# Performance work log

Measured on AMD Instinct MI355X. Metric: run time of the kernel, lower is better.

## Reference

```python
import jax, jax.numpy as jnp
import numpy as np

B, S, D = 4, 2048, 2048
NQ, NKV = 16, 4
HD = D // NQ          # head_size = 128
GROUP = NQ // NKV     # 4


def _rope_table(seq_len, head_size, theta=10000.0):
    # [seq, head_size/2, 2] = (cos, sin), matching torch polar freqs_cis
    inv = 1.0 / (theta ** (np.arange(0, head_size, 2, dtype=np.float32) / head_size))
    ang = np.arange(seq_len, dtype=np.float32)[:, None] * inv[None, :]
    return jnp.asarray(np.stack([np.cos(ang), np.sin(ang)], axis=-1))


def setup_inputs() -> dict:
    key = jax.random.key(0)
    ks = jax.random.split(key, 6)
    sd = 0.02
    return {
        "x": jax.random.normal(ks[0], (B, S, D), jnp.float32),
        "freq_cis": _rope_table(S, HD),
        "Wq": jax.random.normal(ks[1], (D, NQ * HD), jnp.float32) * sd,
        "bq": jnp.zeros((NQ * HD,), jnp.float32),
        "Wk": jax.random.normal(ks[2], (D, NKV * HD), jnp.float32) * sd,
        "bk": jnp.zeros((NKV * HD,), jnp.float32),
        "Wv": jax.random.normal(ks[3], (D, NKV * HD), jnp.float32) * sd,
        "bv": jnp.zeros((NKV * HD,), jnp.float32),
        "Wo": jax.random.normal(ks[4], (NQ * HD, D), jnp.float32) * sd,
        "start_pos": 0,
    }


def _apply_rope(x, fc):
    # x: [b, s, h, d]; fc: [s, d/2, 2] -> complex multiply on (even, odd) pairs
    xr = x.reshape(*x.shape[:-1], -1, 2)
    cos = fc[None, :, None, :, 0]
    sin = fc[None, :, None, :, 1]
    x0, x1 = xr[..., 0], xr[..., 1]
    out = jnp.stack([x0 * cos - x1 * sin, x0 * sin + x1 * cos], axis=-1)
    return out.reshape(x.shape)


def reference(x, freq_cis, Wq, bq, Wk, bk, Wv, bv, Wo, start_pos):
    b, s, _ = x.shape
    q = (x @ Wq + bq).reshape(b, s, NQ, HD)
    k = (x @ Wk + bk).reshape(b, s, NKV, HD)
    v = (x @ Wv + bv).reshape(b, s, NKV, HD)

    fc = freq_cis[start_pos:start_pos + s]
    q = _apply_rope(q, fc)
    k = _apply_rope(k, fc)

    # [b, nkv, group, s, d] query view; k/v stay [b, nkv, s, d] (GQA broadcast)
    q = q.transpose(0, 2, 1, 3).reshape(b, NKV, GROUP, s, HD)
    k = k.transpose(0, 2, 1, 3)
    v = v.transpose(0, 2, 1, 3)

    scale = 1.0 / jnp.sqrt(jnp.asarray(HD, x.dtype))
    scores = jnp.einsum("bhgqd,bhkd->bhgqk", q, k) * scale
    causal = jnp.tril(jnp.ones((s, s), bool))
    scores = jnp.where(causal[None, None, None], scores, jnp.asarray(-jnp.inf, scores.dtype))
    probs = jax.nn.softmax(scores, axis=-1)
    o = jnp.einsum("bhgqk,bhkd->bhgqd", probs, v)

    o = o.reshape(b, NQ, s, HD).transpose(0, 2, 1, 3).reshape(b, s, NQ * HD)
    return o @ Wo
```

## Files before the change

### kernel.cpp

```cpp
#include <hip/hip_runtime.h>
#include <stdint.h>

typedef __attribute__((ext_vector_type(8))) short bf16x8;
typedef __attribute__((ext_vector_type(4))) float f32x4;
typedef __attribute__((ext_vector_type(16))) float f32x16;

#define S_LEN 2048
#define D_MODEL 2048
#define NQH 16
#define NKVH 4
#define HDIM 128
#define BATCH 4

__device__ __forceinline__ float bf2f(unsigned short s) {
  union { unsigned u; float f; } v; v.u = ((unsigned)s) << 16; return v.f;
}
__device__ __forceinline__ unsigned short f2bf(float f) {
  union { float f; unsigned u; } v; v.f = f;
  unsigned r = v.u + 0x7FFFu + ((v.u >> 16) & 1u);
  return (unsigned short)(r >> 16);
}
__device__ __forceinline__ f32x4 fzero() {
  f32x4 v; v[0]=0.f; v[1]=0.f; v[2]=0.f; v[3]=0.f; return v;
}
__device__ __forceinline__ void async16(const void* g, void* l) {
  __builtin_amdgcn_global_load_lds(
      (const __attribute__((address_space(1))) unsigned int*)g,
      (__attribute__((address_space(3))) unsigned int*)l, 16, 0, 0);
}
__device__ __forceinline__ unsigned cvtpk(float lo, float hi) {
  unsigned r;
  asm("v_cvt_pk_bf16_f32 %0, %1, %2" : "=v"(r) : "v"(lo), "v"(hi));
  return r;
}

__global__ void k_convert_x(const float* __restrict__ x, unsigned short* __restrict__ xb, int n4) {
  int stride = gridDim.x * blockDim.x;
  for (int i = blockIdx.x * blockDim.x + threadIdx.x; i < n4; i += stride) {
    float4 v = ((const float4*)x)[i];
    ushort4 o;
    o.x = f2bf(v.x); o.y = f2bf(v.y); o.z = f2bf(v.z); o.w = f2bf(v.w);
    ((ushort4*)xb)[i] = o;
  }
}

__global__ void k_transpose_convert(const float* __restrict__ W, unsigned short* __restrict__ Wt,
                                    int K, int N) {
  __shared__ float tile[32][33];
  int tx = threadIdx.x & 31, ty = threadIdx.x >> 5;
  int n0 = blockIdx.x * 32, k0 = blockIdx.y * 32;
  #pragma unroll
  for (int i = 0; i < 4; ++i)
    tile[ty + i*8][tx] = W[(size_t)(k0 + ty + i*8) * N + n0 + tx];
  __syncthreads();
  #pragma unroll
  for (int i = 0; i < 4; ++i)
    Wt[(size_t)(n0 + ty + i*8) * K + k0 + tx] = f2bf(tile[tx][ty + i*8]);
}

__global__ void k_transpose_bf16(const unsigned short* __restrict__ src,
                                 unsigned short* __restrict__ dst, int R, int C) {
  __shared__ unsigned short tile[32][33];
  int tx = threadIdx.x & 31, ty = threadIdx.x >> 5;
  int c0 = blockIdx.x * 32, r0 = blockIdx.y * 32;
  const unsigned short* s = src + (size_t)blockIdx.z * R * C;
  unsigned short* d = dst + (size_t)blockIdx.z * R * C;
  #pragma unroll
  for (int i = 0; i < 4; ++i)
    tile[ty + i*8][tx] = s[(size_t)(r0 + ty + i*8) * C + c0 + tx];
  __syncthreads();
  #pragma unroll
  for (int i = 0; i < 4; ++i)
    d[(size_t)(c0 + ty + i*8) * R + r0 + tx] = tile[tx][ty + i*8];
}

#define BARRIER() __builtin_amdgcn_s_barrier()
#define LGKM0()  do { asm volatile("s_waitcnt lgkmcnt(0)" ::: "memory"); \
                      __builtin_amdgcn_sched_barrier(0); } while (0)
#define VMCNT6() asm volatile("s_waitcnt vmcnt(6)" ::: "memory")
#define VMCNT4() asm volatile("s_waitcnt vmcnt(4)" ::: "memory")
#define VMCNT0() asm volatile("s_waitcnt vmcnt(0)" ::: "memory")

__device__ __forceinline__ bf16x8 ldsrd(const unsigned short* L, int row, int kk, int g) {
  int Xs = (kk * 64 + g * 16) ^ ((row & 7) << 4);
  return *(const bf16x8*)&L[row * 64 + (Xs >> 1)];
}
__device__ __forceinline__ void stage8(const unsigned short* __restrict__ G, int gbase,
                                       int k0, unsigned short* lds, int rowbase, int lane) {
  int row = rowbase + (lane >> 3);
  int col8 = (lane & 7) ^ ((lane >> 3) & 7);
  async16(G + (size_t)(gbase + row) * 2048 + k0 + col8 * 8, lds + rowbase * 64 + lane * 8);
}

__global__ __launch_bounds__(512, 2) void k_gemm_qkv(
    const unsigned short* __restrict__ A, const unsigned short* __restrict__ Bt,
    const float* __restrict__ bq, const float* __restrict__ bk, const float* __restrict__ bv,
    const float* __restrict__ fc, const int* __restrict__ start_pos,
    unsigned short* __restrict__ Qo, unsigned short* __restrict__ Ko, unsigned short* __restrict__ Vo)
{
  __shared__ __align__(16) unsigned short Ab[3][256 * 64];
  __shared__ __align__(16) unsigned short Bb[3][128 * 64];
  const int NT = 32, NXT = 24;
  const int tid = threadIdx.x, lane = tid & 63, w = tid >> 6;
  const int lr = lane & 15, g = lane >> 4;
  const int wm = w >> 2, wn = w & 3;

  int nwg = NXT * 32;
  int cpx = nwg >> 3;
  int bid = blockIdx.x;
  int swz = (bid & 7) * cpx + (bid >> 3);
  const int by = swz / NXT, bx = swz % NXT;
  const int mbase = by * 256, nbase = bx * 128;

  #define ST_A(tt) { unsigned short* L = Ab[(tt) % 3]; int k0 = (tt) * 64; \
    _Pragma("unroll") for (int it = 0; it < 4; ++it) { int c = tid + it * 512; \
      int row = c >> 3, col8 = (c & 7) ^ (row & 7); \
      async16(A + (size_t)(mbase + row) * 2048 + k0 + col8 * 8, L + c * 8); } }
  #define ST_B(tt) { unsigned short* L = Bb[(tt) % 3]; int k0 = (tt) * 64; \
    _Pragma("unroll") for (int it = 0; it < 2; ++it) { int c = tid + it * 512; \
      int row = c >> 3, col8 = (c & 7) ^ (row & 7); \
      async16(Bt + (size_t)(nbase + row) * 2048 + k0 + col8 * 8, L + c * 8); } }

  f32x4 acc[8][2];
  #pragma unroll
  for (int m = 0; m < 8; ++m)
    #pragma unroll
    for (int n = 0; n < 2; ++n) acc[m][n] = fzero();

  ST_A(0); ST_B(0); ST_A(1); ST_B(1);
  VMCNT6();
  BARRIER();

  for (int t = 0; t < NT; ++t) {
    const unsigned short* Al = Ab[t % 3];
    const unsigned short* Bl = Bb[t % 3];
    bf16x8 a[2][4], b[2][2];

    #pragma unroll
    for (int kk = 0; kk < 2; ++kk) {
      #pragma unroll
      for (int m = 0; m < 4; ++m) a[kk][m] = ldsrd(Al, wm * 128 + m * 16 + lr, kk, g);
      #pragma unroll
      for (int n = 0; n < 2; ++n) b[kk][n] = ldsrd(Bl, wn * 32 + n * 16 + lr, kk, g);
    }
    if (t + 2 < NT) ST_A(t + 2);
    BARRIER(); LGKM0();
    __builtin_amdgcn_s_setprio(1);
    #pragma unroll
    for (int kk = 0; kk < 2; ++kk)
      #pragma unroll
      for (int m = 0; m < 4; ++m)
        #pragma unroll
        for (int n = 0; n < 2; ++n)
          acc[m][n] = __builtin_amdgcn_mfma_f32_16x16x32_bf16(a[kk][m], b[kk][n], acc[m][n], 0, 0, 0);
    __builtin_amdgcn_s_setprio(0);
    BARRIER();

    #pragma unroll
    for (int kk = 0; kk < 2; ++kk)
      #pragma unroll
      for (int m = 0; m < 4; ++m) a[kk][m] = ldsrd(Al, wm * 128 + 64 + m * 16 + lr, kk, g);
    if (t + 2 < NT) { ST_B(t + 2); VMCNT6(); } else { VMCNT0(); }
    BARRIER(); LGKM0();
    __builtin_amdgcn_s_setprio(1);
    #pragma unroll
    for (int kk = 0; kk < 2; ++kk)
      #pragma unroll
      for (int m = 0; m < 4; ++m)
        #pragma unroll
        for (int n = 0; n < 2; ++n)
          acc[4 + m][n] = __builtin_amdgcn_mfma_f32_16x16x32_bf16(a[kk][m], b[kk][n], acc[4 + m][n], 0, 0, 0);
    __builtin_amdgcn_s_setprio(0);
    BARRIER();
  }

  const int sp = start_pos[0];
  #pragma unroll
  for (int n = 0; n < 2; ++n) {
    const int ng = nbase + wn * 32 + n * 16 + lr;
    unsigned short* dst;
    int NH; float bias;
    if (ng < 2048)      { dst = Qo; NH = NQH;  bias = bq[ng]; }
    else if (ng < 2560) { dst = Ko; NH = NKVH; bias = bk[ng - 2048]; }
    else                { dst = Vo; NH = NKVH; bias = bv[ng - 2560]; }
    const int hh = (ng < 2048 ? ng : (ng < 2560 ? ng - 2048 : ng - 2560)) >> 7;
    const int dd = ng & 127;
    const bool dorope = (ng < 2560);
    const size_t hoff = (size_t)hh * S_LEN * HDIM + dd;
    const int d2 = dd >> 1;
    #pragma unroll
    for (int m = 0; m < 8; ++m)
      #pragma unroll
      for (int i = 0; i < 4; ++i) {
        int mg = mbase + wm * 128 + (m >> 2) * 64 + (m & 3) * 16 + g * 4 + i;
        int bb = mg >> 11, s = mg & 2047;
        float val = acc[m][n][i] + bias;
        float other = __shfl_xor(val, 1);
        if (dorope) {
          float2 cs = *(const float2*)&fc[((size_t)(sp + s) * 64 + d2) * 2];
          val = (dd & 1) ? fmaf(other, cs.y, val * cs.x)
                         : (val * cs.x - other * cs.y);
        }
        dst[(size_t)bb * NH * S_LEN * HDIM + hoff + (size_t)s * HDIM] = f2bf(val);
      }
  }
  #undef ST_A
  #undef ST_B
}

__global__ __launch_bounds__(512, 2) void k_gemm_out256(
    const unsigned short* __restrict__ A, const unsigned short* __restrict__ Bt,
    float* __restrict__ Cf)
{
  __shared__ __align__(16) unsigned short Abuf[2][256 * 64];
  __shared__ __align__(16) unsigned short Bbuf[2][256 * 64];
  const int NT = 32, NXT = 8;
  const int tid = threadIdx.x, lane = tid & 63, w = tid >> 6;
  const int lr = lane & 15, g = lane >> 4;
  const int wm = w >> 2, wn = w & 3;

  int nwg = NXT * 32;
  int cpx = nwg >> 3;
  int bid = blockIdx.x;
  int swz = (bid & 7) * cpx + (bid >> 3);
  const int by = swz / NXT, bx = swz % NXT;
  const int mbase = by * 256, nbase = bx * 256;

  #define ST_AQ02(tt) if ((tt) < NT) { unsigned short* L = Abuf[(tt) & 1]; int k0 = (tt) * 64; \
    _Pragma("unroll") for (int it = 0; it < 2; ++it) { int sub = it * 8 + w; \
      stage8(A, mbase, k0, L, (sub >> 3) * 128 + (sub & 7) * 8, lane); } }
  #define ST_AQ13(tt) if ((tt) < NT) { unsigned short* L = Abuf[(tt) & 1]; int k0 = (tt) * 64; \
    _Pragma("unroll") for (int it = 0; it < 2; ++it) { int sub = it * 8 + w; \
      stage8(A, mbase, k0, L, 64 + (sub >> 3) * 128 + (sub & 7) * 8, lane); } }
  #define ST_BS0(tt) if ((tt) < NT) { unsigned short* L = Bbuf[(tt) & 1]; int k0 = (tt) * 64; \
    _Pragma("unroll") for (int it = 0; it < 2; ++it) { int sub = it * 8 + w; \
      stage8(Bt, nbase, k0, L, (sub >> 2) * 64 + (sub & 3) * 8, lane); } }
  #define ST_BS1(tt) if ((tt) < NT) { unsigned short* L = Bbuf[(tt) & 1]; int k0 = (tt) * 64; \
    _Pragma("unroll") for (int it = 0; it < 2; ++it) { int sub = it * 8 + w; \
      stage8(Bt, nbase, k0, L, 32 + (sub >> 2) * 64 + (sub & 3) * 8, lane); } }

  f32x4 acc[8][4];
  #pragma unroll
  for (int m = 0; m < 8; ++m)
    #pragma unroll
    for (int n = 0; n < 4; ++n) acc[m][n] = fzero();

  ST_AQ02(0); ST_AQ13(0); ST_BS0(0); ST_BS1(0);
  ST_AQ02(1); ST_BS1(1);
  VMCNT4();
  BARRIER();

  bf16x8 a[2][4], b[2][2];

  for (int t = 0; t < NT; ++t) {
    const unsigned short* Al = Abuf[t & 1];
    const unsigned short* Bl = Bbuf[t & 1];

    #pragma unroll
    for (int kk = 0; kk < 2; ++kk) {
      #pragma unroll
      for (int m = 0; m < 4; ++m) a[kk][m] = ldsrd(Al, wm * 128 + m * 16 + lr, kk, g);
      #pragma unroll
      for (int n = 0; n < 2; ++n) b[kk][n] = ldsrd(Bl, wn * 64 + n * 16 + lr, kk, g);
    }
    ST_AQ13(t + 1);
    BARRIER(); LGKM0();
    __builtin_amdgcn_s_setprio(1);
    #pragma unroll
    for (int kk = 0; kk < 2; ++kk)
      #pragma unroll
      for (int m = 0; m < 4; ++m)
        #pragma unroll
        for (int n = 0; n < 2; ++n)
          acc[m][n] = __builtin_amdgcn_mfma_f32_16x16x32_bf16(a[kk][m], b[kk][n], acc[m][n], 0, 0, 0);
    __builtin_amdgcn_s_setprio(0);
    BARRIER();

    #pragma unroll
    for (int kk = 0; kk < 2; ++kk)
      #pragma unroll
      for (int n = 0; n < 2; ++n) b[kk][n] = ldsrd(Bl, wn * 64 + (2 + n) * 16 + lr, kk, g);
    ST_BS0(t + 1);
    BARRIER(); LGKM0();
    __builtin_amdgcn_s_setprio(1);
    #pragma unroll
    for (int kk = 0; kk < 2; ++kk)
      #pragma unroll
      for (int m = 0; m < 4; ++m)
        #pragma unroll
        for (int n = 0; n < 2; ++n)
          acc[m][2 + n] = __builtin_amdgcn_mfma_f32_16x16x32_bf16(a[kk][m], b[kk][n], acc[m][2 + n], 0, 0, 0);
    __builtin_amdgcn_s_setprio(0);
    BARRIER();

    #pragma unroll
    for (int kk = 0; kk < 2; ++kk)
      #pragma unroll
      for (int m = 0; m < 4; ++m) a[kk][m] = ldsrd(Al, wm * 128 + 64 + m * 16 + lr, kk, g);
    ST_AQ02(t + 2);
    BARRIER(); LGKM0();
    __builtin_amdgcn_s_setprio(1);
    #pragma unroll
    for (int kk = 0; kk < 2; ++kk)
      #pragma unroll
      for (int m = 0; m < 4; ++m)
        #pragma unroll
        for (int n = 0; n < 2; ++n)
          acc[4 + m][2 + n] = __builtin_amdgcn_mfma_f32_16x16x32_bf16(a[kk][m], b[kk][n], acc[4 + m][2 + n], 0, 0, 0);
    __builtin_amdgcn_s_setprio(0);
    BARRIER();

    #pragma unroll
    for (int kk = 0; kk < 2; ++kk)
      #pragma unroll
      for (int n = 0; n < 2; ++n) b[kk][n] = ldsrd(Bl, wn * 64 + n * 16 + lr, kk, g);
    ST_BS1(t + 2);
    VMCNT4();
    BARRIER(); LGKM0();
    __builtin_amdgcn_s_setprio(1);
    #pragma unroll
    for (int kk = 0; kk < 2; ++kk)
      #pragma unroll
      for (int m = 0; m < 4; ++m)
        #pragma unroll
        for (int n = 0; n < 2; ++n)
          acc[4 + m][n] = __builtin_amdgcn_mfma_f32_16x16x32_bf16(a[kk][m], b[kk][n], acc[4 + m][n], 0, 0, 0);
    __builtin_amdgcn_s_setprio(0);
    BARRIER();
  }

  #pragma unroll
  for (int m = 0; m < 8; ++m)
    #pragma unroll
    for (int n = 0; n < 4; ++n)
      #pragma unroll
      for (int i = 0; i < 4; ++i) {
        int mg = mbase + wm * 128 + m * 16 + g * 4 + i;
        int ng = nbase + wn * 64 + n * 16 + lr;
        Cf[(size_t)mg * 2048 + ng] = acc[m][n][i];
      }
  #undef ST_AQ02
  #undef ST_AQ13
  #undef ST_BS0
  #undef ST_BS1
}

__global__ __launch_bounds__(512, 2) void k_flash2(
    const unsigned short* __restrict__ Q, const unsigned short* __restrict__ K,
    const unsigned short* __restrict__ Vt, unsigned short* __restrict__ O)
{
  __shared__ __align__(16) unsigned short SH[32768];

  const int tid = threadIdx.x;
  const int lane = tid & 63;
  const int w = tid >> 6;
  const int ql = lane & 31;
  const int hi = lane >> 5;

  const int bh = blockIdx.x >> 2;
  const int tp = blockIdx.x & 3;
  const int b = bh >> 4, h = bh & 15;
  const int kh = h >> 2;

  const unsigned short* Qbase = Q + (size_t)(b * NQH + h) * S_LEN * HDIM;
  const unsigned short* Kbase = K + (size_t)(b * NKVH + kh) * S_LEN * HDIM;
  const unsigned short* Vtb   = Vt + (size_t)(b * NKVH + kh) * HDIM * S_LEN;

  const float scale = 0.08838834764831845f;

  #pragma unroll 1
  for (int half = 0; half < 2; ++half) {
    const int t = half ? (7 - tp) : tp;
    const int nkv = 4 * t + 4;
    const int qg = t * 256 + w * 32 + ql;

    __syncthreads();

    bf16x8 qf[8];
    {
      const unsigned short* qp = Qbase + (size_t)qg * HDIM;
      #pragma unroll
      for (int dd = 0; dd < 8; ++dd)
        qf[dd] = *(const bf16x8*)(qp + dd * 16 + hi * 8);
    }

    float m_r = -1e30f, l_r = 0.f;
    f32x16 oA[4];
    #pragma unroll
    for (int db = 0; db < 4; ++db)
      #pragma unroll
      for (int r = 0; r < 16; ++r) oA[db][r] = 0.f;

    {
      unsigned short* Kd = SH;
      unsigned short* Vd = SH + 16384;
      #pragma unroll
      for (int it = 0; it < 2; ++it) {
        int c = tid + it * 512;
        int row = c >> 4, col = c & 15;
        int lcol = (col & 8) | ((col ^ (row & 7)) & 7);
        async16(Kbase + (size_t)row * HDIM + lcol * 8, Kd + c * 8);
      }
      #pragma unroll
      for (int it = 0; it < 2; ++it) {
        int c = tid + it * 512;
        int row = c >> 3, col = c & 7;
        int lcol = col ^ (row & 7);
        async16(Vtb + (size_t)row * S_LEN + lcol * 8, Vd + c * 8);
      }
    }
    __syncthreads();

    for (int j = 0; j < nkv; ++j) {
      const int cur = j & 1;
      const unsigned short* Kl = SH + cur * 8192;
      const unsigned short* Vl = SH + 16384 + cur * 8192;

      if (j + 1 < nkv) {
        unsigned short* Kd = SH + (cur ^ 1) * 8192;
        unsigned short* Vd = SH + 16384 + (cur ^ 1) * 8192;
        #pragma unroll
        for (int it = 0; it < 2; ++it) {
          int c = tid + it * 512;
          int row = c >> 4, col = c & 15;
          int lcol = (col & 8) | ((col ^ (row & 7)) & 7);
          async16(Kbase + (size_t)((j + 1) * 64 + row) * HDIM + lcol * 8, Kd + c * 8);
        }
        #pragma unroll
        for (int it = 0; it < 2; ++it) {
          int c = tid + it * 512;
          int row = c >> 3, col = c & 7;
          int lcol = col ^ (row & 7);
          async16(Vtb + (size_t)row * S_LEN + (j + 1) * 64 + lcol * 8, Vd + c * 8);
        }
      }

      if (j * 64 <= t * 256 + w * 32 + 31) {
        f32x16 p0, p1;
        #pragma unroll
        for (int r = 0; r < 16; ++r) { p0[r] = 0.f; p1[r] = 0.f; }
        #pragma unroll
        for (int dd = 0; dd < 8; ++dd) {
          const int off = (((dd * 32 + hi * 16) ^ ((ql & 7) << 4)) >> 1);
          bf16x8 a0 = *(const bf16x8*)&Kl[ql * 128 + off];
          bf16x8 a1 = *(const bf16x8*)&Kl[(32 + ql) * 128 + off];
          p0 = __builtin_amdgcn_mfma_f32_32x32x16_bf16(a0, qf[dd], p0, 0, 0, 0);
          p1 = __builtin_amdgcn_mfma_f32_32x32x16_bf16(a1, qf[dd], p1, 0, 0, 0);
        }

        #pragma unroll
        for (int r = 0; r < 16; ++r) {
          const int kl = (r & 3) + 8 * (r >> 2);
          int kg = j * 64 + kl + 4 * hi;
          p0[r] = (kg > qg) ? -1e30f : p0[r] * scale;
          p1[r] = (kg + 32 > qg) ? -1e30f : p1[r] * scale;
        }

        float pm = -1e30f;
        #pragma unroll
        for (int r = 0; r < 16; ++r) pm = fmaxf(pm, fmaxf(p0[r], p1[r]));
        pm = fmaxf(pm, __shfl_xor(pm, 32));
        const float mn = fmaxf(m_r, pm);
        const float corr = __expf(m_r - mn);
        m_r = mn;
        float rs = 0.f;
        #pragma unroll
        for (int r = 0; r < 16; ++r) {
          p0[r] = __expf(p0[r] - mn);
          p1[r] = __expf(p1[r] - mn);
          rs += p0[r] + p1[r];
        }
        rs += __shfl_xor(rs, 32);
        l_r = l_r * corr + rs;
        #pragma unroll
        for (int db = 0; db < 4; ++db)
          #pragma unroll
          for (int r = 0; r < 16; ++r) oA[db][r] *= corr;

        bf16x8 pb[4];
        {
          unsigned Wv[8], W2v[8];
          #pragma unroll
          for (int d = 0; d < 4; ++d) {
            Wv[d]      = cvtpk(p0[4*d],     p0[4*d + 1]);
            W2v[d]     = cvtpk(p0[4*d + 2], p0[4*d + 3]);
            Wv[4 + d]  = cvtpk(p1[4*d],     p1[4*d + 1]);
            W2v[4 + d] = cvtpk(p1[4*d + 2], p1[4*d + 3]);
          }
          #pragma unroll
          for (int kt = 0; kt < 2; ++kt) {
            #pragma unroll
            for (int s = 0; s < 2; ++s) {
              unsigned ownW   = hi ? Wv[kt*4 + 2*s + 1]  : Wv[kt*4 + 2*s];
              unsigned sendW  = hi ? Wv[kt*4 + 2*s]      : Wv[kt*4 + 2*s + 1];
              unsigned recvW  = (unsigned)__shfl_xor((int)sendW, 32);
              unsigned ownW2  = hi ? W2v[kt*4 + 2*s + 1] : W2v[kt*4 + 2*s];
              unsigned sendW2 = hi ? W2v[kt*4 + 2*s]     : W2v[kt*4 + 2*s + 1];
              unsigned recvW2 = (unsigned)__shfl_xor((int)sendW2, 32);
              union { unsigned u[4]; bf16x8 v; } pk;
              pk.u[0] = hi ? recvW  : ownW;
              pk.u[1] = hi ? recvW2 : ownW2;
              pk.u[2] = hi ? ownW   : recvW;
              pk.u[3] = hi ? ownW2  : recvW2;
              pb[kt*2 + s] = pk.v;
            }
          }
        }

        #pragma unroll
        for (int ks = 0; ks < 4; ++ks) {
          #pragma unroll
          for (int db = 0; db < 4; ++db) {
            const int off = (((ks * 32 + hi * 16) ^ ((ql & 7) << 4)) >> 1);
            bf16x8 av = *(const bf16x8*)&Vl[(db * 32 + ql) * 64 + off];
            oA[db] = __builtin_amdgcn_mfma_f32_32x32x16_bf16(av, pb[ks], oA[db], 0, 0, 0);
          }
        }
      }
      __syncthreads();
    }

    {
      const float invl = 1.f / l_r;
      const int qloc = w * 32 + ql;
      #pragma unroll
      for (int db = 0; db < 4; ++db)
        #pragma unroll
        for (int g4 = 0; g4 < 4; ++g4) {
          unsigned lo  = cvtpk(oA[db][g4*4 + 0] * invl, oA[db][g4*4 + 1] * invl);
          unsigned hi2 = cvtpk(oA[db][g4*4 + 2] * invl, oA[db][g4*4 + 3] * invl);
          int byteoff = qloc * 256 + ((db * 64 + g4 * 16 + hi * 8) ^ ((qloc & 7) << 4));
          *(uint2*)((char*)SH + byteoff) = make_uint2(lo, hi2);
        }
    }
    __syncthreads();
    {
      const int q2 = tid >> 1, hf = tid & 1;
      unsigned short* orow = O + ((size_t)(b * S_LEN + t * 256 + q2)) * D_MODEL + h * HDIM + hf * 64;
      #pragma unroll
      for (int u = 0; u < 8; ++u) {
        int byteoff = q2 * 256 + ((hf * 128 + u * 16) ^ ((q2 & 7) << 4));
        bf16x8 v = *(const bf16x8*)((const char*)SH + byteoff);
        *(bf16x8*)(orow + u * 8) = v;
      }
    }
  }
}

extern "C" void kernel_launch(void* const* d_in, const int* in_sizes, int n_in,
                              void* d_out, int out_size, void* d_ws, size_t ws_size,
                              hipStream_t stream) {
  (void)in_sizes; (void)n_in; (void)out_size; (void)ws_size;
  const float* x  = (const float*)d_in[0];
  const float* fc = (const float*)d_in[1];
  const float* Wq = (const float*)d_in[2];
  const float* bq = (const float*)d_in[3];
  const float* Wk = (const float*)d_in[4];
  const float* bk = (const float*)d_in[5];
  const float* Wv = (const float*)d_in[6];
  const float* bv = (const float*)d_in[7];
  const float* Wo = (const float*)d_in[8];
  const int* start_pos = (const int*)d_in[9];
  float* out = (float*)d_out;

  unsigned short* ws = (unsigned short*)d_ws;
  size_t off = 0;
  unsigned short* xb  = ws + off; off += (size_t)8192 * 2048;
  unsigned short* Wt  = ws + off; off += (size_t)3072 * 2048;
  unsigned short* Wot = ws + off; off += (size_t)2048 * 2048;
  unsigned short* Qb  = ws + off; off += (size_t)BATCH * NQH  * S_LEN * HDIM;
  unsigned short* Kb  = ws + off; off += (size_t)BATCH * NKVH * S_LEN * HDIM;
  unsigned short* Vb  = ws + off; off += (size_t)BATCH * NKVH * S_LEN * HDIM;
  unsigned short* Vtb = ws + off; off += (size_t)BATCH * NKVH * S_LEN * HDIM;
  unsigned short* Ob  = ws + off; off += (size_t)8192 * 2048;

  k_convert_x<<<2048, 256, 0, stream>>>(x, xb, 8192 * 2048 / 4);
  k_transpose_convert<<<dim3(64, 64), 256, 0, stream>>>(Wq, Wt, 2048, 2048);
  k_transpose_convert<<<dim3(16, 64), 256, 0, stream>>>(Wk, Wt + (size_t)2048 * 2048, 2048, 512);
  k_transpose_convert<<<dim3(16, 64), 256, 0, stream>>>(Wv, Wt + (size_t)2560 * 2048, 2048, 512);
  k_transpose_convert<<<dim3(64, 64), 256, 0, stream>>>(Wo, Wot, 2048, 2048);

  k_gemm_qkv<<<dim3(768), 512, 0, stream>>>(xb, Wt, bq, bk, bv, fc, start_pos, Qb, Kb, Vb);

  k_transpose_bf16<<<dim3(4, 64, 16), 256, 0, stream>>>(Vb, Vtb, S_LEN, HDIM);

  k_flash2<<<dim3(256), 512, 0, stream>>>(Qb, Kb, Vtb, Ob);

  k_gemm_out256<<<dim3(256), 512, 0, stream>>>(Ob, Wot, out);
}
```

Baseline: 389.5 us.

## Write V transposed from QKV GEMM, split RoPE out, lazy softmax rescale

The QKV GEMM epilogue now writes V directly in transposed layout, which removes the separate bf16 transpose kernel. It also folds the softmax scale times log2(e) into Q before storing. RoPE moves out of the epilogue into a standalone elementwise pass over Q and K, so Q and K are read and written an extra time. The flash kernel switches to exp2 and only rescales the running max, l and O accumulators when the block max grows by more than 8. The trade is fewer exp and rescale operations in attention against extra memory passes, strided V stores in the epilogue, and an extra bf16 rounding of Q and K.

Result: faster. 374.9 us (-3.7%).

```diff
diff --git a/kernel.cpp b/kernel.cpp
--- a/kernel.cpp
+++ b/kernel.cpp
@@ -58,20 +58,22 @@
     Wt[(size_t)(n0 + ty + i*8) * K + k0 + tx] = f2bf(tile[tx][ty + i*8]);
 }
 
-__global__ void k_transpose_bf16(const unsigned short* __restrict__ src,
-                                 unsigned short* __restrict__ dst, int R, int C) {
-  __shared__ unsigned short tile[32][33];
-  int tx = threadIdx.x & 31, ty = threadIdx.x >> 5;
-  int c0 = blockIdx.x * 32, r0 = blockIdx.y * 32;
-  const unsigned short* s = src + (size_t)blockIdx.z * R * C;
-  unsigned short* d = dst + (size_t)blockIdx.z * R * C;
-  #pragma unroll
-  for (int i = 0; i < 4; ++i)
-    tile[ty + i*8][tx] = s[(size_t)(r0 + ty + i*8) * C + c0 + tx];
-  __syncthreads();
-  #pragma unroll
-  for (int i = 0; i < 4; ++i)
-    d[(size_t)(c0 + ty + i*8) * R + r0 + tx] = tile[tx][ty + i*8];
+__global__ void k_rope(unsigned short* __restrict__ T, const float* __restrict__ fc,
+                       const int* __restrict__ start_pos, int total) {
+  int sp = start_pos[0];
+  int stride = gridDim.x * blockDim.x;
+  for (int i = blockIdx.x * blockDim.x + threadIdx.x; i < total; i += stride) {
+    int d2 = i & 63;
+    int s = (i >> 6) & (S_LEN - 1);
+    unsigned v = ((const unsigned*)T)[i];
+    float x0 = bf2f((unsigned short)(v & 0xFFFFu));
+    float x1 = bf2f((unsigned short)(v >> 16));
+    float c  = fc[((size_t)(sp + s) * 64 + d2) * 2];
+    float sn = fc[((size_t)(sp + s) * 64 + d2) * 2 + 1];
+    float y0 = x0 * c - x1 * sn;
+    float y1 = x0 * sn + x1 * c;
+    ((unsigned*)T)[i] = (unsigned)f2bf(y0) | ((unsigned)f2bf(y1) << 16);
+  }
 }
 
 #define BARRIER() __builtin_amdgcn_s_barrier()
@@ -95,8 +97,7 @@
 __global__ __launch_bounds__(512, 2) void k_gemm_qkv(
     const unsigned short* __restrict__ A, const unsigned short* __restrict__ Bt,
     const float* __restrict__ bq, const float* __restrict__ bk, const float* __restrict__ bv,
-    const float* __restrict__ fc, const int* __restrict__ start_pos,
-    unsigned short* __restrict__ Qo, unsigned short* __restrict__ Ko, unsigned short* __restrict__ Vo)
+    unsigned short* __restrict__ Qo, unsigned short* __restrict__ Ko, unsigned short* __restrict__ Vto)
 {
   __shared__ __align__(16) unsigned short Ab[3][256 * 64];
   __shared__ __align__(16) unsigned short Bb[3][128 * 64];
@@ -174,20 +175,14 @@
     BARRIER();
   }
 
-  const int sp = start_pos[0];
+  const float SCL2E = 0.08838834764831845f * 1.4426950408889634f;
   #pragma unroll
   for (int n = 0; n < 2; ++n) {
     const int ng = nbase + wn * 32 + n * 16 + lr;
-    unsigned short* dst;
-    int NH; float bias;
-    if (ng < 2048)      { dst = Qo; NH = NQH;  bias = bq[ng]; }
-    else if (ng < 2560) { dst = Ko; NH = NKVH; bias = bk[ng - 2048]; }
-    else                { dst = Vo; NH = NKVH; bias = bv[ng - 2560]; }
-    const int hh = (ng < 2048 ? ng : (ng < 2560 ? ng - 2048 : ng - 2560)) >> 7;
-    const int dd = ng & 127;
-    const bool dorope = (ng < 2560);
-    const size_t hoff = (size_t)hh * S_LEN * HDIM + dd;
-    const int d2 = dd >> 1;
+    const int seg = (ng < 2048) ? 0 : (ng < 2560 ? 1 : 2);
+    const int nn = ng - (seg == 0 ? 0 : (seg == 1 ? 2048 : 2560));
+    const int hh = nn >> 7, dd = nn & 127;
+    const float bias = (seg == 0 ? bq[nn] : (seg == 1 ? bk[nn] : bv[nn]));
     #pragma unroll
     for (int m = 0; m < 8; ++m)
       #pragma unroll
@@ -195,13 +190,14 @@
         int mg = mbase + wm * 128 + (m >> 2) * 64 + (m & 3) * 16 + g * 4 + i;
         int bb = mg >> 11, s = mg & 2047;
         float val = acc[m][n][i] + bias;
-        float other = __shfl_xor(val, 1);
-        if (dorope) {
-          float2 cs = *(const float2*)&fc[((size_t)(sp + s) * 64 + d2) * 2];
-          val = (dd & 1) ? fmaf(other, cs.y, val * cs.x)
-                         : (val * cs.x - other * cs.y);
-        }
-        dst[(size_t)bb * NH * S_LEN * HDIM + hoff + (size_t)s * HDIM] = f2bf(val);
+        if (seg == 0) {
+          val *= SCL2E;
+          Qo[((size_t)(bb * NQH + hh) * S_LEN + s) * HDIM + dd] = f2bf(val);
+        } else if (seg == 1) {
+          Ko[((size_t)(bb * NKVH + hh) * S_LEN + s) * HDIM + dd] = f2bf(val);
+        } else {
+          Vto[((size_t)(bb * NKVH + hh) * HDIM + dd) * S_LEN + s] = f2bf(val);
+        }
       }
   }
   #undef ST_A
@@ -366,8 +362,6 @@
   const unsigned short* Kbase = K + (size_t)(b * NKVH + kh) * S_LEN * HDIM;
   const unsigned short* Vtb   = Vt + (size_t)(b * NKVH + kh) * HDIM * S_LEN;
 
-  const float scale = 0.08838834764831845f;
-
   #pragma unroll 1
   for (int half = 0; half < 2; ++half) {
     const int t = half ? (7 - tp) : tp;
@@ -452,30 +446,33 @@
         for (int r = 0; r < 16; ++r) {
           const int kl = (r & 3) + 8 * (r >> 2);
           int kg = j * 64 + kl + 4 * hi;
-          p0[r] = (kg > qg) ? -1e30f : p0[r] * scale;
-          p1[r] = (kg + 32 > qg) ? -1e30f : p1[r] * scale;
+          if (kg > qg) p0[r] = -1e30f;
+          if (kg + 32 > qg) p1[r] = -1e30f;
         }
 
         float pm = -1e30f;
         #pragma unroll
         for (int r = 0; r < 16; ++r) pm = fmaxf(pm, fmaxf(p0[r], p1[r]));
         pm = fmaxf(pm, __shfl_xor(pm, 32));
-        const float mn = fmaxf(m_r, pm);
-        const float corr = __expf(m_r - mn);
-        m_r = mn;
+        if (!__all(pm - m_r <= 8.0f)) {
+          const float mn = fmaxf(m_r, pm);
+          const float corr = exp2f(m_r - mn);
+          m_r = mn;
+          l_r *= corr;
+          #pragma unroll
+          for (int db = 0; db < 4; ++db)
+            #pragma unroll
+            for (int r = 0; r < 16; ++r) oA[db][r] *= corr;
+        }
         float rs = 0.f;
         #pragma unroll
         for (int r = 0; r < 16; ++r) {
-          p0[r] = __expf(p0[r] - mn);
-          p1[r] = __expf(p1[r] - mn);
+          p0[r] = exp2f(p0[r] - m_r);
+          p1[r] = exp2f(p1[r] - m_r);
           rs += p0[r] + p1[r];
         }
         rs += __shfl_xor(rs, 32);
-        l_r = l_r * corr + rs;
-        #pragma unroll
-        for (int db = 0; db < 4; ++db)
-          #pragma unroll
-          for (int r = 0; r < 16; ++r) oA[db][r] *= corr;
+        l_r += rs;
 
         bf16x8 pb[4];
         {
@@ -570,7 +567,6 @@
   unsigned short* Wot = ws + off; off += (size_t)2048 * 2048;
   unsigned short* Qb  = ws + off; off += (size_t)BATCH * NQH  * S_LEN * HDIM;
   unsigned short* Kb  = ws + off; off += (size_t)BATCH * NKVH * S_LEN * HDIM;
-  unsigned short* Vb  = ws + off; off += (size_t)BATCH * NKVH * S_LEN * HDIM;
   unsigned short* Vtb = ws + off; off += (size_t)BATCH * NKVH * S_LEN * HDIM;
   unsigned short* Ob  = ws + off; off += (size_t)8192 * 2048;
 
@@ -580,9 +576,10 @@
   k_transpose_convert<<<dim3(16, 64), 256, 0, stream>>>(Wv, Wt + (size_t)2560 * 2048, 2048, 512);
   k_transpose_convert<<<dim3(64, 64), 256, 0, stream>>>(Wo, Wot, 2048, 2048);
 
-  k_gemm_qkv<<<dim3(768), 512, 0, stream>>>(xb, Wt, bq, bk, bv, fc, start_pos, Qb, Kb, Vb);
-
-  k_transpose_bf16<<<dim3(4, 64, 16), 256, 0, stream>>>(Vb, Vtb, S_LEN, HDIM);
+  k_gemm_qkv<<<dim3(768), 512, 0, stream>>>(xb, Wt, bq, bk, bv, Qb, Kb, Vtb);
+
+  k_rope<<<2048, 256, 0, stream>>>(Qb, fc, start_pos, BATCH * NQH * S_LEN * 64);
+  k_rope<<<2048, 256, 0, stream>>>(Kb, fc, start_pos, BATCH * NKVH * S_LEN * 64);
 
   k_flash2<<<dim3(256), 512, 0, stream>>>(Qb, Kb, Vtb, Ob);
 
```
